# Performance work log

Measured on AMD Instinct MI355X. Metric: run time of the kernel, lower is better.

The kernel has to match this reference:

```python
import jax, jax.numpy as jnp
import numpy as np

N_HEADS = 2
HEAD_DIM = 32
SCALE = HEAD_DIM ** -0.5


def group_linear(x, w):
    # x: (S, B, din), w: (n_blocks, din_b, dout_b) block-diagonal linear
    S, B, _ = x.shape
    nb, din_b, dout_b = w.shape
    xb = x.reshape(S, B, nb, din_b)
    yb = jnp.einsum('sbnd,nde->sbne', xb, w)
    return yb.reshape(S, B, nb * dout_b)


def setup_inputs() -> dict:
    key = jax.random.key(0)
    ks = jax.random.split(key, 5)
    S, B, dim, nb = 2048, 16, 1024, 8
    block_din = dim // nb          # 128
    emb_b = HEAD_DIM * N_HEADS     # 64 per block
    x = jax.random.normal(ks[0], (S, B, dim), dtype=jnp.float32)
    wq = 0.01 * jax.random.normal(ks[1], (nb, block_din, emb_b), dtype=jnp.float32)
    wk = 0.01 * jax.random.normal(ks[2], (nb, block_din, emb_b), dtype=jnp.float32)
    wv = 0.01 * jax.random.normal(ks[3], (nb, block_din, emb_b), dtype=jnp.float32)
    wf = 0.01 * jax.random.normal(ks[4], (nb, emb_b, block_din), dtype=jnp.float32)
    return {'x': x, 'wq': wq, 'wk': wk, 'wv': wv, 'wf': wf}


def reference(x, wq, wk, wv, wf):
    S, B, dim = x.shape
    nb = wq.shape[0]
    # block-diagonal QKV projections -> (S, B, nb, n_heads, head_dim)
    q = group_linear(x, wq).reshape(S, B, nb, N_HEADS, HEAD_DIM)
    k = group_linear(x, wk).reshape(S, B, nb, N_HEADS, HEAD_DIM)
    v = group_linear(x, wv).reshape(S, B, nb, N_HEADS, HEAD_DIM)
    # attention over the n_blocks axis; heads leading: (S, B, h, nb, hd)
    q = jnp.swapaxes(q, 2, 3) * SCALE
    k = jnp.swapaxes(k, 2, 3)
    v = jnp.swapaxes(v, 2, 3)
    score = jnp.einsum('sbhnd,sbhmd->sbhnm', q, k)  # (S,B,h,nb,nb)
    score = jax.nn.softmax(score, axis=-1)
    out = jnp.einsum('sbhnm,sbhmd->sbhnd', score, v)
    out = jnp.swapaxes(out, 2, 3).reshape(S, B, nb * N_HEADS * HEAD_DIM)
    out = group_linear(out, wf)
    return out.reshape(S, B, dim)
```

## Files before the change

### kernel.cpp

```cpp
#include <hip/hip_runtime.h>
#include <math.h>

using short8  = __attribute__((ext_vector_type(8))) short;
using ushort8 = __attribute__((ext_vector_type(8))) unsigned short;
using f32x4   = __attribute__((ext_vector_type(4))) float;

constexpr int DIM = 1024, NB = 8, NH = 2, HD = 32;
constexpr float SCALE = 0.17677669529663687f;
constexpr int SXW = 1032;
constexpr int SQW = 1544;

__device__ __forceinline__ unsigned short f2bf(float f) {
  unsigned u = __float_as_uint(f);
  u += 0x7fff + ((u >> 16) & 1);
  return (unsigned short)(u >> 16);
}
__device__ __forceinline__ float bf2f(unsigned short h) {
  return __uint_as_float((unsigned)h << 16);
}
__device__ __forceinline__ unsigned pack2bf(float lo, float hi) {
  return (unsigned)f2bf(lo) | ((unsigned)f2bf(hi) << 16);
}

__device__ __forceinline__ int qk_off(int R, int blk, int sub) {
  return R * 32 + ((blk ^ (R & 3)) * 8) + sub;
}

__global__ __launch_bounds__(256) void prep_weights(
    const float* __restrict__ wq, const float* __restrict__ wk,
    const float* __restrict__ wv, const float* __restrict__ wf,
    unsigned short* __restrict__ ws)
{
  int gid = blockIdx.x * 256 + threadIdx.x;
  if (gid < 196608) {
    int t = gid >> 11, r = gid & 2047;
    int s = r >> 9, l = (r >> 3) & 63, z = r & 7;
    int met = t >> 3, n = t & 7, m = met >> 2, et = met & 3;
    int fr = l & 15, fg = l >> 4;
    int e = et * 16 + fr, k = s * 32 + fg * 8 + z;
    const float* w = (m == 0) ? wq : (m == 1) ? wk : wv;
    float v = w[n * 8192 + k * 64 + e];
    if (m == 0) v *= SCALE;
    ws[gid] = f2bf(v);
  } else {
    int g2 = gid - 196608;
    int t = g2 >> 10, r = g2 & 1023;
    int s = r >> 9, l = (r >> 3) & 63, z = r & 7;
    int n = t >> 3, et = t & 7;
    int fr = l & 15, fg = l >> 4;
    int eo = et * 16 + fr, k = s * 32 + fg * 8 + z;
    ws[gid] = f2bf(wf[n * 8192 + k * 128 + eo]);
  }
}

__global__ __launch_bounds__(512, 4) void gc_fused(
    const float* __restrict__ x,
    const unsigned short* __restrict__ wsw,
    const unsigned short* __restrict__ wsf,
    float* __restrict__ out)
{
  __shared__ __align__(16) unsigned short smem[16 * SQW];

  const int tid  = threadIdx.x;
  const int lane = tid & 63;
  const int w    = tid >> 6;
  const int fr   = lane & 15;
  const int fg   = lane >> 4;
  const long tok0 = (long)blockIdx.x * 16;

  {
    const float* xb = x + tok0 * DIM;
    float4 xa[4], xc[4];
    #pragma unroll
    for (int jj = 0; jj < 4; ++jj) {
      int chunk = tid + 512 * jj;
      const float* src = xb + (long)(chunk >> 7) * DIM + (chunk & 127) * 8;
      xa[jj] = *reinterpret_cast<const float4*>(src);
      xc[jj] = *reinterpret_cast<const float4*>(src + 4);
    }
    #pragma unroll
    for (int jj = 0; jj < 4; ++jj) {
      int chunk = tid + 512 * jj;
      ushort8 v;
      v[0] = f2bf(xa[jj].x); v[1] = f2bf(xa[jj].y);
      v[2] = f2bf(xa[jj].z); v[3] = f2bf(xa[jj].w);
      v[4] = f2bf(xc[jj].x); v[5] = f2bf(xc[jj].y);
      v[6] = f2bf(xc[jj].z); v[7] = f2bf(xc[jj].w);
      *reinterpret_cast<ushort8*>(&smem[(chunk >> 7) * SXW + (chunk & 127) * 8]) = v;
    }
  }
  __syncthreads();

  ushort4 qreg[12];
  {
    short8 wfrag[4][4];
    #pragma unroll
    for (int p = 0; p < 4; ++p) {
      const unsigned short* wp = wsw + (w * 12 + p) * 2048 + lane * 8;
      #pragma unroll
      for (int s = 0; s < 4; ++s)
        wfrag[p][s] = *reinterpret_cast<const short8*>(wp + s * 512);
    }
    #pragma unroll
    for (int j = 0; j < 12; ++j) {
      const int n = (w * 12 + j) & 7;
      short8 bfr[4];
      #pragma unroll
      for (int s = 0; s < 4; ++s)
        bfr[s] = *reinterpret_cast<const short8*>(&smem[fr * SXW + n * 128 + s * 32 + fg * 8]);
      f32x4 acc = {0.f, 0.f, 0.f, 0.f};
      #pragma unroll
      for (int s = 0; s < 4; ++s)
        acc = __builtin_amdgcn_mfma_f32_16x16x32_bf16(wfrag[j & 3][s], bfr[s], acc, 0, 0, 0);
      if (j + 4 < 12) {
        const unsigned short* wp = wsw + (w * 12 + j + 4) * 2048 + lane * 8;
        #pragma unroll
        for (int s = 0; s < 4; ++s)
          wfrag[j & 3][s] = *reinterpret_cast<const short8*>(wp + s * 512);
      }
      ushort4 d4;
      d4.x = f2bf(acc[0]); d4.y = f2bf(acc[1]);
      d4.z = f2bf(acc[2]); d4.w = f2bf(acc[3]);
      qreg[j] = d4;
    }
  }
  __syncthreads();

  {
    #pragma unroll
    for (int j = 0; j < 12; ++j) {
      const int cc = w * 12 + j;
      const int met = cc >> 3, n = cc & 7;
      const int m = met >> 2, e0 = (met & 3) * 16;
      if (m < 2) {
        const int e00 = e0 + fg * 4;
        const int h = e00 >> 5, dd0 = e00 & 31;
        const int R = 2 * n + h;
        *reinterpret_cast<ushort4*>(
            &smem[fr * SQW + m * 512 + qk_off(R, dd0 >> 3, dd0 & 7)]) = qreg[j];
      } else {
        const unsigned short vals[4] = {qreg[j].x, qreg[j].y, qreg[j].z, qreg[j].w};
        #pragma unroll
        for (int r = 0; r < 4; ++r) {
          const int e = e0 + fg * 4 + r, dd = e & 31, h = e >> 5;
          smem[fr * SQW + 1024 + h * 256 + dd * 8 + n] = vals[r];
        }
      }
    }
  }
  __syncthreads();

  {
    const int la = lane & 15, ga = lane >> 4;
    const int R  = 2 * (la & 7) + (la >> 3);
    const int qoff = qk_off(R, ga, 0);
    const bool useful = ((ga >> 1) == (la >> 3));
    const bool kvalid = (ga < 2);
    const int srcA = (ga * 32 + la) & 63;
    #pragma unroll
    for (int tt = 0; tt < 2; ++tt) {
      const int t = w * 2 + tt;
      const unsigned short* tb = &smem[t * SQW];
      short8 kfr = *reinterpret_cast<const short8*>(tb + 512 + qoff);
      short8 qfr = *reinterpret_cast<const short8*>(tb + qoff);
      f32x4 zero = {0.f, 0.f, 0.f, 0.f};
      f32x4 s = __builtin_amdgcn_mfma_f32_16x16x32_bf16(kfr, qfr, zero, 0, 0, 0);
      float m4 = fmaxf(fmaxf(s[0], s[1]), fmaxf(s[2], s[3]));
      float mx = fmaxf(m4, __shfl_xor(m4, 16));
      float e0 = __expf(s[0] - mx), e1 = __expf(s[1] - mx);
      float e2 = __expf(s[2] - mx), e3 = __expf(s[3] - mx);
      float sm  = e0 + e1 + e2 + e3;
      float smt = sm + __shfl_xor(sm, 16);
      float inv = useful ? (1.f / smt) : 0.f;
      unsigned pk01 = pack2bf(e0 * inv, e1 * inv);
      unsigned pk23 = pack2bf(e2 * inv, e3 * inv);
      unsigned b0 = (unsigned)__builtin_amdgcn_ds_bpermute(srcA * 4, (int)pk01);
      unsigned b1 = (unsigned)__builtin_amdgcn_ds_bpermute(srcA * 4, (int)pk23);
      unsigned b2 = (unsigned)__builtin_amdgcn_ds_bpermute(((srcA + 16) & 63) * 4, (int)pk01);
      unsigned b3 = (unsigned)__builtin_amdgcn_ds_bpermute(((srcA + 16) & 63) * 4, (int)pk23);
      union { unsigned u[4]; short8 s8; } pb;
      pb.u[0] = kvalid ? b0 : 0u;  pb.u[1] = kvalid ? b1 : 0u;
      pb.u[2] = kvalid ? b2 : 0u;  pb.u[3] = kvalid ? b3 : 0u;
      #pragma unroll
      for (int dh = 0; dh < 2; ++dh) {
        short8 va = *reinterpret_cast<const short8*>(
            tb + 1024 + (ga & 1) * 256 + (dh * 16 + la) * 8);
        f32x4 o = __builtin_amdgcn_mfma_f32_16x16x32_bf16(va, pb.s8, zero, 0, 0, 0);
        ushort4 ou;
        ou.x = f2bf(o[0]); ou.y = f2bf(o[1]); ou.z = f2bf(o[2]); ou.w = f2bf(o[3]);
        const int blk = 2 * dh + (ga >> 1);
        *reinterpret_cast<ushort4*>(
            &smem[t * SQW + qk_off(R, blk, (ga & 1) * 4)]) = ou;
      }
    }
  }
  __syncthreads();

  {
    const int n = w;
    short8 wfd[8][2];
    #pragma unroll
    for (int et = 0; et < 8; ++et) {
      const unsigned short* wp = wsf + (n * 8 + et) * 1024 + lane * 8;
      wfd[et][0] = *reinterpret_cast<const short8*>(wp);
      wfd[et][1] = *reinterpret_cast<const short8*>(wp + 512);
    }
    short8 bfr[2];
    #pragma unroll
    for (int s = 0; s < 2; ++s) {
      const int R = 2 * n + s;
      bfr[s] = *reinterpret_cast<const short8*>(&smem[fr * SQW + qk_off(R, fg, 0)]);
    }
    #pragma unroll
    for (int et = 0; et < 8; ++et) {
      f32x4 acc = {0.f, 0.f, 0.f, 0.f};
      #pragma unroll
      for (int s = 0; s < 2; ++s)
        acc = __builtin_amdgcn_mfma_f32_16x16x32_bf16(wfd[et][s], bfr[s], acc, 0, 0, 0);
      float4 o; o.x = acc[0]; o.y = acc[1]; o.z = acc[2]; o.w = acc[3];
      *reinterpret_cast<float4*>(out + (tok0 + fr) * DIM + n * 128 + et * 16 + fg * 4) = o;
    }
  }
}

extern "C" void kernel_launch(void* const* d_in, const int* in_sizes, int n_in,
                              void* d_out, int out_size, void* d_ws, size_t ws_size,
                              hipStream_t stream) {
  const float* x  = (const float*)d_in[0];
  const float* wq = (const float*)d_in[1];
  const float* wk = (const float*)d_in[2];
  const float* wv = (const float*)d_in[3];
  const float* wf = (const float*)d_in[4];
  float* out = (float*)d_out;
  unsigned short* ws = (unsigned short*)d_ws;

  prep_weights<<<dim3(1024), dim3(256), 0, stream>>>(wq, wk, wv, wf, ws);

  const int tokens = in_sizes[0] / DIM;
  gc_fused<<<dim3(tokens / 16), dim3(512), 0, stream>>>(x, ws, ws + 196608, out);
}
```

Baseline: 90.39 us.

## Process 32 tokens per block to reuse weight fragments across two MFMA tiles

Doubles the token tile per workgroup from 16 to 32, so each loaded weight fragment feeds two MFMAs in both the QKV and output projections. This halves global weight traffic per token. Weight prefetching drops from a 4-deep to a 2-deep buffer, and the attention loop now handles 4 tokens per wave. The cost is twice the LDS (SQW padding is also removed), occupancy lowered to 2 blocks per CU, and more register pressure.

Measured after the change: 125.5 us. 38.9% more time.

```diff
diff --git a/kernel.cpp b/kernel.cpp
--- a/kernel.cpp
+++ b/kernel.cpp
@@ -6,9 +6,10 @@
 using f32x4   = __attribute__((ext_vector_type(4))) float;
 
 constexpr int DIM = 1024, NB = 8, NH = 2, HD = 32;
+constexpr int T   = 32;
 constexpr float SCALE = 0.17677669529663687f;
 constexpr int SXW = 1032;
-constexpr int SQW = 1544;
+constexpr int SQW = 1536;
 
 __device__ __forceinline__ unsigned short f2bf(float f) {
   unsigned u = __float_as_uint(f);
@@ -53,33 +54,33 @@
   }
 }
 
-__global__ __launch_bounds__(512, 4) void gc_fused(
+__global__ __launch_bounds__(512, 2) void gc_fused(
     const float* __restrict__ x,
     const unsigned short* __restrict__ wsw,
     const unsigned short* __restrict__ wsf,
     float* __restrict__ out)
 {
-  __shared__ __align__(16) unsigned short smem[16 * SQW];
+  __shared__ __align__(16) unsigned short smem[T * SQW];
 
   const int tid  = threadIdx.x;
   const int lane = tid & 63;
   const int w    = tid >> 6;
   const int fr   = lane & 15;
   const int fg   = lane >> 4;
-  const long tok0 = (long)blockIdx.x * 16;
+  const long tok0 = (long)blockIdx.x * T;
 
   {
     const float* xb = x + tok0 * DIM;
-    float4 xa[4], xc[4];
-    #pragma unroll
-    for (int jj = 0; jj < 4; ++jj) {
+    float4 xa[8], xc[8];
+    #pragma unroll
+    for (int jj = 0; jj < 8; ++jj) {
       int chunk = tid + 512 * jj;
       const float* src = xb + (long)(chunk >> 7) * DIM + (chunk & 127) * 8;
       xa[jj] = *reinterpret_cast<const float4*>(src);
       xc[jj] = *reinterpret_cast<const float4*>(src + 4);
     }
     #pragma unroll
-    for (int jj = 0; jj < 4; ++jj) {
+    for (int jj = 0; jj < 8; ++jj) {
       int chunk = tid + 512 * jj;
       ushort8 v;
       v[0] = f2bf(xa[jj].x); v[1] = f2bf(xa[jj].y);
@@ -91,37 +92,39 @@
   }
   __syncthreads();
 
-  ushort4 qreg[12];
-  {
-    short8 wfrag[4][4];
-    #pragma unroll
-    for (int p = 0; p < 4; ++p) {
-      const unsigned short* wp = wsw + (w * 12 + p) * 2048 + lane * 8;
-      #pragma unroll
-      for (int s = 0; s < 4; ++s)
-        wfrag[p][s] = *reinterpret_cast<const short8*>(wp + s * 512);
-    }
+  ushort4 qreg[12][2];
+  {
+    short8 wfr[2][4];
+    const unsigned short* wp0 = wsw + (w * 12) * 2048 + lane * 8;
+    #pragma unroll
+    for (int s = 0; s < 4; ++s)
+      wfr[0][s] = *reinterpret_cast<const short8*>(wp0 + s * 512);
     #pragma unroll
     for (int j = 0; j < 12; ++j) {
-      const int n = (w * 12 + j) & 7;
-      short8 bfr[4];
-      #pragma unroll
-      for (int s = 0; s < 4; ++s)
-        bfr[s] = *reinterpret_cast<const short8*>(&smem[fr * SXW + n * 128 + s * 32 + fg * 8]);
-      f32x4 acc = {0.f, 0.f, 0.f, 0.f};
-      #pragma unroll
-      for (int s = 0; s < 4; ++s)
-        acc = __builtin_amdgcn_mfma_f32_16x16x32_bf16(wfrag[j & 3][s], bfr[s], acc, 0, 0, 0);
-      if (j + 4 < 12) {
-        const unsigned short* wp = wsw + (w * 12 + j + 4) * 2048 + lane * 8;
+      const int cc = w * 12 + j;
+      const int n  = cc & 7;
+      if (j < 11) {
+        const unsigned short* wpn = wsw + (cc + 1) * 2048 + lane * 8;
         #pragma unroll
         for (int s = 0; s < 4; ++s)
-          wfrag[j & 3][s] = *reinterpret_cast<const short8*>(wp + s * 512);
-      }
-      ushort4 d4;
-      d4.x = f2bf(acc[0]); d4.y = f2bf(acc[1]);
-      d4.z = f2bf(acc[2]); d4.w = f2bf(acc[3]);
-      qreg[j] = d4;
+          wfr[(j + 1) & 1][s] = *reinterpret_cast<const short8*>(wpn + s * 512);
+      }
+      short8 b0[4], b1[4];
+      #pragma unroll
+      for (int s = 0; s < 4; ++s) {
+        b0[s] = *reinterpret_cast<const short8*>(&smem[fr * SXW + n * 128 + s * 32 + fg * 8]);
+        b1[s] = *reinterpret_cast<const short8*>(&smem[(fr + 16) * SXW + n * 128 + s * 32 + fg * 8]);
+      }
+      f32x4 a0 = {0.f, 0.f, 0.f, 0.f}, a1 = {0.f, 0.f, 0.f, 0.f};
+      #pragma unroll
+      for (int s = 0; s < 4; ++s) {
+        a0 = __builtin_amdgcn_mfma_f32_16x16x32_bf16(wfr[j & 1][s], b0[s], a0, 0, 0, 0);
+        a1 = __builtin_amdgcn_mfma_f32_16x16x32_bf16(wfr[j & 1][s], b1[s], a1, 0, 0, 0);
+      }
+      qreg[j][0].x = f2bf(a0[0]); qreg[j][0].y = f2bf(a0[1]);
+      qreg[j][0].z = f2bf(a0[2]); qreg[j][0].w = f2bf(a0[3]);
+      qreg[j][1].x = f2bf(a1[0]); qreg[j][1].y = f2bf(a1[1]);
+      qreg[j][1].z = f2bf(a1[2]); qreg[j][1].w = f2bf(a1[3]);
     }
   }
   __syncthreads();
@@ -132,18 +135,23 @@
       const int cc = w * 12 + j;
       const int met = cc >> 3, n = cc & 7;
       const int m = met >> 2, e0 = (met & 3) * 16;
-      if (m < 2) {
-        const int e00 = e0 + fg * 4;
-        const int h = e00 >> 5, dd0 = e00 & 31;
-        const int R = 2 * n + h;
-        *reinterpret_cast<ushort4*>(
-            &smem[fr * SQW + m * 512 + qk_off(R, dd0 >> 3, dd0 & 7)]) = qreg[j];
-      } else {
-        const unsigned short vals[4] = {qreg[j].x, qreg[j].y, qreg[j].z, qreg[j].w};
-        #pragma unroll
-        for (int r = 0; r < 4; ++r) {
-          const int e = e0 + fg * 4 + r, dd = e & 31, h = e >> 5;
-          smem[fr * SQW + 1024 + h * 256 + dd * 8 + n] = vals[r];
+      #pragma unroll
+      for (int u = 0; u < 2; ++u) {
+        const int row = u * 16 + fr;
+        if (m < 2) {
+          const int e00 = e0 + fg * 4;
+          const int h = e00 >> 5, dd0 = e00 & 31;
+          const int R = 2 * n + h;
+          *reinterpret_cast<ushort4*>(
+              &smem[row * SQW + m * 512 + qk_off(R, dd0 >> 3, dd0 & 7)]) = qreg[j][u];
+        } else {
+          const unsigned short vals[4] = {qreg[j][u].x, qreg[j][u].y,
+                                          qreg[j][u].z, qreg[j][u].w};
+          #pragma unroll
+          for (int r = 0; r < 4; ++r) {
+            const int e = e0 + fg * 4 + r, dd = e & 31, h = e >> 5;
+            smem[row * SQW + 1024 + h * 256 + dd * 8 + n] = vals[r];
+          }
         }
       }
     }
@@ -158,8 +166,8 @@
     const bool kvalid = (ga < 2);
     const int srcA = (ga * 32 + la) & 63;
     #pragma unroll
-    for (int tt = 0; tt < 2; ++tt) {
-      const int t = w * 2 + tt;
+    for (int tt = 0; tt < 4; ++tt) {
+      const int t = w * 4 + tt;
       const unsigned short* tb = &smem[t * SQW];
       short8 kfr = *reinterpret_cast<const short8*>(tb + 512 + qoff);
       short8 qfr = *reinterpret_cast<const short8*>(tb + qoff);
@@ -198,27 +206,29 @@
 
   {
     const int n = w;
-    short8 wfd[8][2];
+    short8 bfr[2][2];
+    #pragma unroll
+    for (int u = 0; u < 2; ++u)
+      #pragma unroll
+      for (int s = 0; s < 2; ++s) {
+        const int R = 2 * n + s;
+        bfr[u][s] = *reinterpret_cast<const short8*>(
+            &smem[(u * 16 + fr) * SQW + qk_off(R, fg, 0)]);
+      }
     #pragma unroll
     for (int et = 0; et < 8; ++et) {
       const unsigned short* wp = wsf + (n * 8 + et) * 1024 + lane * 8;
-      wfd[et][0] = *reinterpret_cast<const short8*>(wp);
-      wfd[et][1] = *reinterpret_cast<const short8*>(wp + 512);
-    }
-    short8 bfr[2];
-    #pragma unroll
-    for (int s = 0; s < 2; ++s) {
-      const int R = 2 * n + s;
-      bfr[s] = *reinterpret_cast<const short8*>(&smem[fr * SQW + qk_off(R, fg, 0)]);
-    }
-    #pragma unroll
-    for (int et = 0; et < 8; ++et) {
-      f32x4 acc = {0.f, 0.f, 0.f, 0.f};
-      #pragma unroll
-      for (int s = 0; s < 2; ++s)
-        acc = __builtin_amdgcn_mfma_f32_16x16x32_bf16(wfd[et][s], bfr[s], acc, 0, 0, 0);
-      float4 o; o.x = acc[0]; o.y = acc[1]; o.z = acc[2]; o.w = acc[3];
-      *reinterpret_cast<float4*>(out + (tok0 + fr) * DIM + n * 128 + et * 16 + fg * 4) = o;
+      short8 wfd0 = *reinterpret_cast<const short8*>(wp);
+      short8 wfd1 = *reinterpret_cast<const short8*>(wp + 512);
+      #pragma unroll
+      for (int u = 0; u < 2; ++u) {
+        f32x4 acc = {0.f, 0.f, 0.f, 0.f};
+        acc = __builtin_amdgcn_mfma_f32_16x16x32_bf16(wfd0, bfr[u][0], acc, 0, 0, 0);
+        acc = __builtin_amdgcn_mfma_f32_16x16x32_bf16(wfd1, bfr[u][1], acc, 0, 0, 0);
+        float4 o; o.x = acc[0]; o.y = acc[1]; o.z = acc[2]; o.w = acc[3];
+        *reinterpret_cast<float4*>(
+            out + (tok0 + u * 16 + fr) * DIM + n * 128 + et * 16 + fg * 4) = o;
+      }
     }
   }
 }
@@ -237,5 +247,5 @@
   prep_weights<<<dim3(1024), dim3(256), 0, stream>>>(wq, wk, wv, wf, ws);
 
   const int tokens = in_sizes[0] / DIM;
-  gc_fused<<<dim3(tokens / 16), dim3(512), 0, stream>>>(x, ws, ws + 196608, out);
-}
+  gc_fused<<<dim3(tokens / T), dim3(512), 0, stream>>>(x, ws, ws + 196608, out);
+}
```

## Load x directly into MFMA fragments per block and drop x staging in LDS

Applied to the files above, without the earlier changes.

Each wave now owns one block n, loads its 16x128 slice of x straight from global memory into B fragments and converts to bf16 in registers. This removes the x staging area in LDS, one barrier, and the register array of QKV results that was held until a later scatter. QKV results are written to LDS right after each MFMA, and weight fragments are double-buffered. With less LDS (row stride cut to 1536) and launch bounds raised to 6 blocks, the goal is higher occupancy. The trade-offs are less coalesced global reads of x (32-byte pieces per lane) and bank conflicts from the unpadded stride.

Result: slower. 108.5 us (+20.0%).

```diff
diff --git a/kernel.cpp b/kernel.cpp
--- a/kernel.cpp
+++ b/kernel.cpp
@@ -7,8 +7,7 @@
 
 constexpr int DIM = 1024, NB = 8, NH = 2, HD = 32;
 constexpr float SCALE = 0.17677669529663687f;
-constexpr int SXW = 1032;
-constexpr int SQW = 1544;
+constexpr int SQW = 1536;
 
 __device__ __forceinline__ unsigned short f2bf(float f) {
   unsigned u = __float_as_uint(f);
@@ -53,7 +52,7 @@
   }
 }
 
-__global__ __launch_bounds__(512, 4) void gc_fused(
+__global__ __launch_bounds__(512, 6) void gc_fused(
     const float* __restrict__ x,
     const unsigned short* __restrict__ wsw,
     const unsigned short* __restrict__ wsf,
@@ -66,84 +65,58 @@
   const int w    = tid >> 6;
   const int fr   = lane & 15;
   const int fg   = lane >> 4;
+  const int n    = w;
   const long tok0 = (long)blockIdx.x * 16;
 
-  {
-    const float* xb = x + tok0 * DIM;
-    float4 xa[4], xc[4];
-    #pragma unroll
-    for (int jj = 0; jj < 4; ++jj) {
-      int chunk = tid + 512 * jj;
-      const float* src = xb + (long)(chunk >> 7) * DIM + (chunk & 127) * 8;
-      xa[jj] = *reinterpret_cast<const float4*>(src);
-      xc[jj] = *reinterpret_cast<const float4*>(src + 4);
-    }
-    #pragma unroll
-    for (int jj = 0; jj < 4; ++jj) {
-      int chunk = tid + 512 * jj;
-      ushort8 v;
-      v[0] = f2bf(xa[jj].x); v[1] = f2bf(xa[jj].y);
-      v[2] = f2bf(xa[jj].z); v[3] = f2bf(xa[jj].w);
-      v[4] = f2bf(xc[jj].x); v[5] = f2bf(xc[jj].y);
-      v[6] = f2bf(xc[jj].z); v[7] = f2bf(xc[jj].w);
-      *reinterpret_cast<ushort8*>(&smem[(chunk >> 7) * SXW + (chunk & 127) * 8]) = v;
-    }
-  }
-  __syncthreads();
-
-  ushort4 qreg[12];
-  {
-    short8 wfrag[4][4];
-    #pragma unroll
-    for (int p = 0; p < 4; ++p) {
-      const unsigned short* wp = wsw + (w * 12 + p) * 2048 + lane * 8;
-      #pragma unroll
-      for (int s = 0; s < 4; ++s)
-        wfrag[p][s] = *reinterpret_cast<const short8*>(wp + s * 512);
-    }
+  short8 bfr[4];
+  {
+    const float* xp = x + (tok0 + fr) * DIM + n * 128 + fg * 8;
+    #pragma unroll
+    for (int s = 0; s < 4; ++s) {
+      float4 a = *reinterpret_cast<const float4*>(xp + s * 32);
+      float4 c = *reinterpret_cast<const float4*>(xp + s * 32 + 4);
+      short8 v;
+      v[0] = (short)f2bf(a.x); v[1] = (short)f2bf(a.y);
+      v[2] = (short)f2bf(a.z); v[3] = (short)f2bf(a.w);
+      v[4] = (short)f2bf(c.x); v[5] = (short)f2bf(c.y);
+      v[6] = (short)f2bf(c.z); v[7] = (short)f2bf(c.w);
+      bfr[s] = v;
+    }
+  }
+
+  {
+    short8 wfr[2][4];
+    const unsigned short* wp0 = wsw + (0 * 8 + n) * 2048 + lane * 8;
+    #pragma unroll
+    for (int s = 0; s < 4; ++s)
+      wfr[0][s] = *reinterpret_cast<const short8*>(wp0 + s * 512);
     #pragma unroll
     for (int j = 0; j < 12; ++j) {
-      const int n = (w * 12 + j) & 7;
-      short8 bfr[4];
-      #pragma unroll
-      for (int s = 0; s < 4; ++s)
-        bfr[s] = *reinterpret_cast<const short8*>(&smem[fr * SXW + n * 128 + s * 32 + fg * 8]);
+      if (j < 11) {
+        const unsigned short* wpn = wsw + ((j + 1) * 8 + n) * 2048 + lane * 8;
+        #pragma unroll
+        for (int s = 0; s < 4; ++s)
+          wfr[(j + 1) & 1][s] = *reinterpret_cast<const short8*>(wpn + s * 512);
+      }
       f32x4 acc = {0.f, 0.f, 0.f, 0.f};
       #pragma unroll
       for (int s = 0; s < 4; ++s)
-        acc = __builtin_amdgcn_mfma_f32_16x16x32_bf16(wfrag[j & 3][s], bfr[s], acc, 0, 0, 0);
-      if (j + 4 < 12) {
-        const unsigned short* wp = wsw + (w * 12 + j + 4) * 2048 + lane * 8;
-        #pragma unroll
-        for (int s = 0; s < 4; ++s)
-          wfrag[j & 3][s] = *reinterpret_cast<const short8*>(wp + s * 512);
-      }
-      ushort4 d4;
-      d4.x = f2bf(acc[0]); d4.y = f2bf(acc[1]);
-      d4.z = f2bf(acc[2]); d4.w = f2bf(acc[3]);
-      qreg[j] = d4;
-    }
-  }
-  __syncthreads();
-
-  {
-    #pragma unroll
-    for (int j = 0; j < 12; ++j) {
-      const int cc = w * 12 + j;
-      const int met = cc >> 3, n = cc & 7;
-      const int m = met >> 2, e0 = (met & 3) * 16;
+        acc = __builtin_amdgcn_mfma_f32_16x16x32_bf16(wfr[j & 1][s], bfr[s], acc, 0, 0, 0);
+      const int m = j >> 2, e0 = (j & 3) * 16;
       if (m < 2) {
+        ushort4 d4;
+        d4.x = f2bf(acc[0]); d4.y = f2bf(acc[1]);
+        d4.z = f2bf(acc[2]); d4.w = f2bf(acc[3]);
         const int e00 = e0 + fg * 4;
         const int h = e00 >> 5, dd0 = e00 & 31;
         const int R = 2 * n + h;
         *reinterpret_cast<ushort4*>(
-            &smem[fr * SQW + m * 512 + qk_off(R, dd0 >> 3, dd0 & 7)]) = qreg[j];
+            &smem[fr * SQW + m * 512 + qk_off(R, dd0 >> 3, dd0 & 7)]) = d4;
       } else {
-        const unsigned short vals[4] = {qreg[j].x, qreg[j].y, qreg[j].z, qreg[j].w};
         #pragma unroll
         for (int r = 0; r < 4; ++r) {
           const int e = e0 + fg * 4 + r, dd = e & 31, h = e >> 5;
-          smem[fr * SQW + 1024 + h * 256 + dd * 8 + n] = vals[r];
+          smem[fr * SQW + 1024 + h * 256 + dd * 8 + n] = f2bf(acc[r]);
         }
       }
     }
@@ -197,26 +170,20 @@
   __syncthreads();
 
   {
-    const int n = w;
-    short8 wfd[8][2];
+    short8 bfr2[2];
+    #pragma unroll
+    for (int s = 0; s < 2; ++s) {
+      const int R = 2 * n + s;
+      bfr2[s] = *reinterpret_cast<const short8*>(&smem[fr * SQW + qk_off(R, fg, 0)]);
+    }
     #pragma unroll
     for (int et = 0; et < 8; ++et) {
       const unsigned short* wp = wsf + (n * 8 + et) * 1024 + lane * 8;
-      wfd[et][0] = *reinterpret_cast<const short8*>(wp);
-      wfd[et][1] = *reinterpret_cast<const short8*>(wp + 512);
-    }
-    short8 bfr[2];
-    #pragma unroll
-    for (int s = 0; s < 2; ++s) {
-      const int R = 2 * n + s;
-      bfr[s] = *reinterpret_cast<const short8*>(&smem[fr * SQW + qk_off(R, fg, 0)]);
-    }
-    #pragma unroll
-    for (int et = 0; et < 8; ++et) {
+      short8 wfd0 = *reinterpret_cast<const short8*>(wp);
+      short8 wfd1 = *reinterpret_cast<const short8*>(wp + 512);
       f32x4 acc = {0.f, 0.f, 0.f, 0.f};
-      #pragma unroll
-      for (int s = 0; s < 2; ++s)
-        acc = __builtin_amdgcn_mfma_f32_16x16x32_bf16(wfd[et][s], bfr[s], acc, 0, 0, 0);
+      acc = __builtin_amdgcn_mfma_f32_16x16x32_bf16(wfd0, bfr2[0], acc, 0, 0, 0);
+      acc = __builtin_amdgcn_mfma_f32_16x16x32_bf16(wfd1, bfr2[1], acc, 0, 0, 0);
       float4 o; o.x = acc[0]; o.y = acc[1]; o.z = acc[2]; o.w = acc[3];
       *reinterpret_cast<float4*>(out + (tok0 + fr) * DIM + n * 128 + et * 16 + fg * 4) = o;
     }
```

## Remap QKV tiles so each wave owns one block, cutting registers for occupancy

Applied to the files above, without the earlier changes.

Each wave now handles all 12 QKV output tiles of a single block (n = wave index) instead of a strided mix of blocks. The x fragments are loaded from LDS once rather than once per tile. Weight fragments are double-buffered with 2 slots instead of 4, and the output-projection weights are loaded per tile instead of all up front. These cuts in register pressure allow launch bounds of 6 blocks per CU, but the shallower prefetch exposes more global-load latency and may cause spills.

Measured after the change: 110.4 us. +22.2%, slower.

```diff
diff --git a/kernel.cpp b/kernel.cpp
--- a/kernel.cpp
+++ b/kernel.cpp
@@ -53,7 +53,7 @@
   }
 }
 
-__global__ __launch_bounds__(512, 4) void gc_fused(
+__global__ __launch_bounds__(512, 6) void gc_fused(
     const float* __restrict__ x,
     const unsigned short* __restrict__ wsw,
     const unsigned short* __restrict__ wsf,
@@ -66,6 +66,7 @@
   const int w    = tid >> 6;
   const int fr   = lane & 15;
   const int fg   = lane >> 4;
+  const int n    = w;
   const long tok0 = (long)blockIdx.x * 16;
 
   {
@@ -93,31 +94,27 @@
 
   ushort4 qreg[12];
   {
-    short8 wfrag[4][4];
-    #pragma unroll
-    for (int p = 0; p < 4; ++p) {
-      const unsigned short* wp = wsw + (w * 12 + p) * 2048 + lane * 8;
-      #pragma unroll
-      for (int s = 0; s < 4; ++s)
-        wfrag[p][s] = *reinterpret_cast<const short8*>(wp + s * 512);
-    }
+    short8 bfr[4];
+    #pragma unroll
+    for (int s = 0; s < 4; ++s)
+      bfr[s] = *reinterpret_cast<const short8*>(&smem[fr * SXW + n * 128 + s * 32 + fg * 8]);
+    short8 wfr[2][4];
+    const unsigned short* wp0 = wsw + n * 2048 + lane * 8;
+    #pragma unroll
+    for (int s = 0; s < 4; ++s)
+      wfr[0][s] = *reinterpret_cast<const short8*>(wp0 + s * 512);
     #pragma unroll
     for (int j = 0; j < 12; ++j) {
-      const int n = (w * 12 + j) & 7;
-      short8 bfr[4];
-      #pragma unroll
-      for (int s = 0; s < 4; ++s)
-        bfr[s] = *reinterpret_cast<const short8*>(&smem[fr * SXW + n * 128 + s * 32 + fg * 8]);
+      if (j < 11) {
+        const unsigned short* wpn = wsw + ((j + 1) * 8 + n) * 2048 + lane * 8;
+        #pragma unroll
+        for (int s = 0; s < 4; ++s)
+          wfr[(j + 1) & 1][s] = *reinterpret_cast<const short8*>(wpn + s * 512);
+      }
       f32x4 acc = {0.f, 0.f, 0.f, 0.f};
       #pragma unroll
       for (int s = 0; s < 4; ++s)
-        acc = __builtin_amdgcn_mfma_f32_16x16x32_bf16(wfrag[j & 3][s], bfr[s], acc, 0, 0, 0);
-      if (j + 4 < 12) {
-        const unsigned short* wp = wsw + (w * 12 + j + 4) * 2048 + lane * 8;
-        #pragma unroll
-        for (int s = 0; s < 4; ++s)
-          wfrag[j & 3][s] = *reinterpret_cast<const short8*>(wp + s * 512);
-      }
+        acc = __builtin_amdgcn_mfma_f32_16x16x32_bf16(wfr[j & 1][s], bfr[s], acc, 0, 0, 0);
       ushort4 d4;
       d4.x = f2bf(acc[0]); d4.y = f2bf(acc[1]);
       d4.z = f2bf(acc[2]); d4.w = f2bf(acc[3]);
@@ -129,9 +126,7 @@
   {
     #pragma unroll
     for (int j = 0; j < 12; ++j) {
-      const int cc = w * 12 + j;
-      const int met = cc >> 3, n = cc & 7;
-      const int m = met >> 2, e0 = (met & 3) * 16;
+      const int m = j >> 2, e0 = (j & 3) * 16;
       if (m < 2) {
         const int e00 = e0 + fg * 4;
         const int h = e00 >> 5, dd0 = e00 & 31;
@@ -197,26 +192,20 @@
   __syncthreads();
 
   {
-    const int n = w;
-    short8 wfd[8][2];
+    short8 bfr2[2];
+    #pragma unroll
+    for (int s = 0; s < 2; ++s) {
+      const int R = 2 * n + s;
+      bfr2[s] = *reinterpret_cast<const short8*>(&smem[fr * SQW + qk_off(R, fg, 0)]);
+    }
     #pragma unroll
     for (int et = 0; et < 8; ++et) {
       const unsigned short* wp = wsf + (n * 8 + et) * 1024 + lane * 8;
-      wfd[et][0] = *reinterpret_cast<const short8*>(wp);
-      wfd[et][1] = *reinterpret_cast<const short8*>(wp + 512);
-    }
-    short8 bfr[2];
-    #pragma unroll
-    for (int s = 0; s < 2; ++s) {
-      const int R = 2 * n + s;
-      bfr[s] = *reinterpret_cast<const short8*>(&smem[fr * SQW + qk_off(R, fg, 0)]);
-    }
-    #pragma unroll
-    for (int et = 0; et < 8; ++et) {
+      short8 wfd0 = *reinterpret_cast<const short8*>(wp);
+      short8 wfd1 = *reinterpret_cast<const short8*>(wp + 512);
       f32x4 acc = {0.f, 0.f, 0.f, 0.f};
-      #pragma unroll
-      for (int s = 0; s < 2; ++s)
-        acc = __builtin_amdgcn_mfma_f32_16x16x32_bf16(wfd[et][s], bfr[s], acc, 0, 0, 0);
+      acc = __builtin_amdgcn_mfma_f32_16x16x32_bf16(wfd0, bfr2[0], acc, 0, 0, 0);
+      acc = __builtin_amdgcn_mfma_f32_16x16x32_bf16(wfd1, bfr2[1], acc, 0, 0, 0);
       float4 o; o.x = acc[0]; o.y = acc[1]; o.z = acc[2]; o.w = acc[3];
       *reinterpret_cast<float4*>(out + (tok0 + fr) * DIM + n * 128 + et * 16 + fg * 4) = o;
     }
```
